# Performance work log

Hardware: AMD Instinct MI355X
Metric: run time of the kernel (lower is better)

## Reference

```python
import jax, jax.numpy as jnp
import numpy as np

NUM_CLASSES = 80
TOP_K = 200
CONF_T = 0.05
NMS_T = 0.5
CROP = 300.0
A = 49104
B = 8
NEG = -1.0  # dead-score sentinel; real scores are sigmoid outputs in (0,1)


def setup_inputs() -> dict:
    key = jax.random.key(0)
    k1, k2, k3, k4, k5, k6 = jax.random.split(key, 6)
    # structured, plausible anchors in (ymin, xmin, ymax, xmax), pixel coords
    yc = jax.random.uniform(k1, (A,)) * CROP
    xc = jax.random.uniform(k2, (A,)) * CROP
    h = 10.0 + jax.random.uniform(k5, (A,)) * 90.0
    w = 10.0 + jax.random.uniform(k6, (A,)) * 90.0
    anchors = jnp.stack([yc - h / 2, xc - w / 2, yc + h / 2, xc + w / 2], axis=-1)
    confidences = jax.random.normal(k3, (B, A, NUM_CLASSES + 1), dtype=jnp.float32)
    regressions = jax.random.normal(k4, (B, A, 4), dtype=jnp.float32) * 0.1
    return {"confidences": confidences, "regressions": regressions, "anchors": anchors}


def _decode(regressions, anchors):
    yca = (anchors[:, 0] + anchors[:, 2]) / 2
    xca = (anchors[:, 1] + anchors[:, 3]) / 2
    ha = anchors[:, 2] - anchors[:, 0]
    wa = anchors[:, 3] - anchors[:, 1]
    w = jnp.exp(regressions[..., 3]) * wa
    h = jnp.exp(regressions[..., 2]) * ha
    yc = regressions[..., 0] * ha + yca
    xc = regressions[..., 1] * wa + xca
    # clamp exactly as the original: min-clamp on xmin/ymin, max-clamp on xmax/ymax
    xmin = jnp.maximum(xc - w / 2, 0.0) / CROP
    ymin = jnp.maximum(yc - h / 2, 0.0) / CROP
    xmax = jnp.minimum(xc + w / 2, CROP - 1.0) / CROP
    ymax = jnp.minimum(yc + h / 2, CROP - 1.0) / CROP
    return jnp.stack([xmin, ymin, xmax, ymax], axis=-1)  # [B,A,4] (x1,y1,x2,y2)


def _iou_one_to_many(box, boxes):
    x1 = jnp.maximum(box[0], boxes[:, 0])
    y1 = jnp.maximum(box[1], boxes[:, 1])
    x2 = jnp.minimum(box[2], boxes[:, 2])
    y2 = jnp.minimum(box[3], boxes[:, 3])
    inter = jnp.maximum(x2 - x1, 0.0) * jnp.maximum(y2 - y1, 0.0)
    area_b = (box[2] - box[0]) * (box[3] - box[1])
    areas = (boxes[:, 2] - boxes[:, 0]) * (boxes[:, 3] - boxes[:, 1])
    union = area_b + areas - inter
    return jnp.where(union > 0, inter / union, 0.0)


def _nms_image(boxes, probs):
    # boxes: [A,4], probs: [A,C] (sigmoid, background stripped)
    scores = jnp.max(probs, axis=1)
    classes = jnp.argmax(probs, axis=1)
    valid = scores > CONF_T
    # batched_nms trick: offset boxes per class so cross-class IoU is 0
    offset = classes.astype(boxes.dtype) * (jnp.max(boxes) + 1.0)
    boxes_o = boxes + offset[:, None]
    live = jnp.where(valid, scores, NEG)

    def body(live, _):
        idx = jnp.argmax(live)
        keep = live[idx] > 0.0
        iou = _iou_one_to_many(boxes_o[idx], boxes_o)
        live = jnp.where(keep & (iou > NMS_T), NEG, live)
        live = live.at[idx].set(NEG)
        return live, (idx, keep)

    _, (idxs, keeps) = jax.lax.scan(body, live, None, length=TOP_K)
    cls_k = classes[idxs]          # [TOP_K]
    sc_k = scores[idxs]            # [TOP_K]
    bx_k = boxes[idxs]             # [TOP_K,4]
    # per-class slot = rank among kept detections of the same class (keep order is score-descending)
    onehot = (cls_k[:, None] == jnp.arange(NUM_CLASSES)[None, :]) & keeps[:, None]
    slot = jnp.cumsum(onehot, axis=0)[jnp.arange(TOP_K), cls_k] - 1
    rows = jnp.where(keeps, cls_k + 1, NUM_CLASSES + 1)  # OOB row when dropped
    slot = jnp.where(keeps, slot, TOP_K)                 # OOB col when dropped
    vals = jnp.concatenate([sc_k[:, None], bx_k], axis=1)  # [TOP_K,5]
    out = jnp.zeros((NUM_CLASSES + 1, TOP_K, 5), boxes.dtype)
    return out.at[rows, slot].set(vals, mode="drop")


def reference(confidences, regressions, anchors):
    probs = jax.nn.sigmoid(confidences[:, :, 1:])
    boxes = _decode(regressions, anchors)
    return jax.vmap(_nms_image)(boxes, probs)  # [B, C+1, TOP_K, 5]
```

## Files before the change

### kernel.cpp

```cpp
#include <hip/hip_runtime.h>
#include <stdint.h>

#define NCLS 80
#define TOPK 200
#define CONF_T 0.05f
#define CROPF 300.0f
#define NA 49104
#define NB 8
#define NSEL 256
#define MKEYS 4096
#define APB 48
#define T1 192
#define CHUNK (APB * 81)
#define NGRP (NA / 16)
#define MROW 5
#define OUTFLO ((NCLS + 1) * TOPK * 5)
#define NBLK1 ((NB * NA) / APB)
#define BASE13 125542u
#define NBINS 4512

__device__ __forceinline__ void decode_box(const float4 rg, const float4 an,
                                           float& x1, float& y1, float& x2, float& y2) {
    float yca = (an.x + an.z) * 0.5f;
    float xca = (an.y + an.w) * 0.5f;
    float ha = an.z - an.x;
    float wa = an.w - an.y;
    float w = expf(rg.w) * wa;
    float h = expf(rg.z) * ha;
    float yc = rg.x * ha + yca;
    float xc = rg.y * wa + xca;
    x1 = fmaxf(xc - w * 0.5f, 0.0f) / CROPF;
    y1 = fmaxf(yc - h * 0.5f, 0.0f) / CROPF;
    x2 = fminf(xc + w * 0.5f, CROPF - 1.0f) / CROPF;
    y2 = fminf(yc + h * 0.5f, CROPF - 1.0f) / CROPF;
}

__device__ __forceinline__ float rlf(float v, int l) {
    return __int_as_float(__builtin_amdgcn_readlane(__float_as_int(v), l));
}

__global__ __launch_bounds__(T1) void phase1_kernel(
    const float* __restrict__ conf, const float* __restrict__ reg,
    const float* __restrict__ anch, float* __restrict__ scores,
    unsigned char* __restrict__ cls, float2* __restrict__ gm2,
    float* __restrict__ outz)
{
    __shared__ float lds[CHUNK];
    const int blk = blockIdx.x, t = threadIdx.x;

    {
        const int gid = blk * T1 + t;
        constexpr int TOT4 = NB * OUTFLO / 4;
        if (gid < TOT4)
            reinterpret_cast<float4*>(outz)[gid] = make_float4(0.f, 0.f, 0.f, 0.f);
    }

    const float4* src = reinterpret_cast<const float4*>(conf + (size_t)blk * CHUNK);
    float4* dst = reinterpret_cast<float4*>(lds);
    for (int i = t; i < CHUNK / 4; i += T1) dst[i] = src[i];
    __syncthreads();

    const int la = t >> 2, sub = t & 3;
    const int quad = blk * APB + la;
    const float* crow = lds + la * 81;
    float best = -3.0e38f; int bc = 255;
    #pragma unroll
    for (int k = 0; k < 20; ++k) {
        int c = 1 + sub + 4 * k;
        float v = crow[c];
        if (v > best) { best = v; bc = c; }
    }
    for (int m = 1; m <= 2; m <<= 1) {
        float ov = __shfl_xor(best, m);
        int oc = __shfl_xor(bc, m);
        if (ov > best || (ov == best && oc < bc)) { best = ov; bc = oc; }
    }
    float bmaxl = 0.0f;
    if (sub == 0) {
        scores[quad] = 1.0f / (1.0f + expf(-best));
        cls[quad] = (unsigned char)(bc - 1);
        int a = quad % NA;
        float4 rg = reinterpret_cast<const float4*>(reg)[quad];
        float4 an = reinterpret_cast<const float4*>(anch)[a];
        float x1, y1, x2, y2; decode_box(rg, an, x1, y1, x2, y2);
        bmaxl = fmaxf(fmaxf(x1, y1), fmaxf(x2, y2));
    }
    float wbest = best;
    #pragma unroll
    for (int m = 1; m < 64; m <<= 1) {
        wbest = fmaxf(wbest, __shfl_xor(wbest, m));
        bmaxl = fmaxf(bmaxl, __shfl_xor(bmaxl, m));
    }
    if ((t & 63) == 0)
        gm2[blk * 3 + (t >> 6)] = make_float2(1.0f / (1.0f + expf(-wbest)), bmaxl);
}

__device__ __forceinline__ void suffix_scan_1024(uint32_t v, int t,
                                                 uint32_t* wtot, uint32_t* outarr) {
    uint32_t r = v;
    const int lane = t & 63, w = t >> 6;
    #pragma unroll
    for (int m = 1; m < 64; m <<= 1) {
        uint32_t o = __shfl_down(r, m);
        if (lane + m < 64) r += o;
    }
    if (lane == 0) wtot[w] = r;
    __syncthreads();
    if (t < 16) {
        uint32_t v0 = wtot[t], x = v0;
        #pragma unroll
        for (int m = 1; m < 16; m <<= 1) {
            uint32_t o = __shfl_down(x, m);
            if (t + m < 16) x += o;
        }
        wtot[t] = x - v0;
    }
    __syncthreads();
    outarr[t] = r + wtot[w];
    __syncthreads();
}

__global__ __launch_bounds__(1024) void phase2_kernel(
    const float* __restrict__ reg, const float* __restrict__ anch,
    const float* __restrict__ scores, const unsigned char* __restrict__ cls,
    const float2* __restrict__ gm2, float* __restrict__ out)
{
    __shared__ uint64_t s_keys[MKEYS];
    __shared__ uint64_t s_skeys[MKEYS];
    __shared__ uint64_t s_mask[256 * MROW];
    __shared__ float4   s_boxo[256];
    __shared__ float    s_areao[256];
    __shared__ float    s_gm[NGRP + 3];
    __shared__ uint32_t s_glist[2048];
    __shared__ float4   s_keptbox[TOPK];
    __shared__ uint64_t s_clsmask[NCLS][4];
    __shared__ uint32_t s_ccount[NCLS];
    __shared__ uint32_t s_wtot[16];
    __shared__ uint32_t s_shv[12];
    __shared__ float    s_bmaxarr[16];
    __shared__ float    s_offm;
    __shared__ uint8_t  s_clsl[256];
    __shared__ uint64_t s_K[4], s_newK[4];
    __shared__ uint32_t s_chg;

    uint32_t* hist = (uint32_t*)s_keys;
    uint32_t* csum = (uint32_t*)s_skeys;

    const int b = blockIdx.x;
    const int t = threadIdx.x;

    for (int i = t; i < NBINS; i += 1024) hist[i] = 0;
    if (t < 12) s_shv[t] = 0;
    __syncthreads();

    {
        const float2* gmb = gm2 + (size_t)b * NGRP;
        float wm = 0.0f;
        for (int i = t; i < NGRP; i += 1024) {
            float2 v = gmb[i];
            s_gm[i] = v.x;
            wm = fmaxf(wm, v.y);
            if (v.x > CONF_T) {
                int ib = (int)((__float_as_uint(v.x) >> 13) - BASE13);
                ib = max(0, min(NBINS - 1, ib));
                atomicAdd(&hist[ib], 1u);
            }
        }
        #pragma unroll
        for (int m = 1; m < 64; m <<= 1) wm = fmaxf(wm, __shfl_xor(wm, m));
        if ((t & 63) == 0) s_bmaxarr[t >> 6] = wm;
    }
    __syncthreads();

    uint32_t v8 = 0;
    if (t * 8 < NBINS) {
        #pragma unroll
        for (int k = 0; k < 8; ++k) v8 += hist[t * 8 + k];
    }
    suffix_scan_1024(v8, t, s_wtot, csum);
    {
        uint32_t sIn = csum[t];
        uint32_t sNext = (t == 1023) ? 0u : csum[t + 1];
        if (sIn >= NSEL && sNext < NSEL) { s_shv[0] = (uint32_t)t; s_shv[1] = sNext; s_shv[2] = 1; }
    }
    __syncthreads();
    if (t == 0) {
        float mx = s_bmaxarr[0];
        #pragma unroll
        for (int k = 1; k < 16; ++k) mx = fmaxf(mx, s_bmaxarr[k]);
        s_offm = mx + 1.0f;
        if (s_shv[2]) {
            uint32_t chunk = s_shv[0], run2 = s_shv[1]; int cb = -1;
            for (int k = 7; k >= 0; --k) {
                uint32_t v = hist[chunk * 8 + k];
                if (cb < 0 && run2 + v >= NSEL) cb = (int)(chunk * 8 + k);
                run2 += v;
            }
            s_shv[3] = BASE13 + (uint32_t)cb;
        } else s_shv[3] = 0;
    }
    __syncthreads();

    const uint32_t T13 = s_shv[3];
    for (int i = t; i < NGRP; i += 1024) {
        float s = s_gm[i];
        if (s > CONF_T && (__float_as_uint(s) >> 13) >= T13) {
            uint32_t p = atomicAdd(&s_shv[8], 1u);
            if (p < 2048u) s_glist[p] = (uint32_t)i;
        }
    }
    __syncthreads();
    uint32_t ngl = s_shv[8]; if (ngl > 2048u) ngl = 2048u;

    {
        const float4* sc4 = reinterpret_cast<const float4*>(scores + (size_t)b * NA);
        #define GATH1(s, g) { if ((s) > CONF_T) { uint32_t _b = __float_as_uint(s); \
            if ((_b >> 13) >= T13) { uint32_t _p = atomicAdd(&s_shv[4], 1u); \
                if (_p < MKEYS) s_keys[_p] = ((uint64_t)_b << 32) | \
                    (uint64_t)(0xFFFFFFFFu - (uint32_t)(g)); } } }
        for (int idx = t; idx < (int)(ngl * 4); idx += 1024) {
            uint32_t gi = s_glist[idx >> 2];
            int q = idx & 3;
            float4 s4 = sc4[gi * 4 + q];
            uint32_t g0 = gi * 16 + (uint32_t)q * 4;
            GATH1(s4.x, g0)     GATH1(s4.y, g0 + 1)
            GATH1(s4.z, g0 + 2) GATH1(s4.w, g0 + 3)
        }
    }
    __syncthreads();
    uint32_t nGa = s_shv[4]; if (nGa > MKEYS) nGa = MKEYS;
    const int lim = (nGa < 256u) ? (int)nGa : 256;

    {
        const int lane = t & 63;
        const uint32_t nch = (nGa + 63) >> 6;
        for (int s = 0; s < 4; ++s) {
            int kid = t + s * 1024;
            bool act = kid < (int)nGa;
            if (__ballot(act) == 0ull) continue;
            uint64_t my = act ? s_keys[kid] : ~0ull;
            uint32_t r = 0;
            for (uint32_t ch = 0; ch < nch; ++ch) {
                uint32_t src = ch * 64 + (uint32_t)lane;
                uint64_t kc = (src < nGa) ? s_keys[src] : 0ull;
                uint32_t clo = (uint32_t)kc, chi = (uint32_t)(kc >> 32);
                for (int jj = 0; jj < 64; ++jj) {
                    uint32_t olo = (uint32_t)__builtin_amdgcn_readlane((int)clo, jj);
                    uint32_t ohi = (uint32_t)__builtin_amdgcn_readlane((int)chi, jj);
                    uint64_t ok = ((uint64_t)ohi << 32) | olo;
                    r += (ok > my) ? 1u : 0u;
                }
            }
            if (act) s_skeys[r] = my;
        }
    }
    __syncthreads();

    const float offm = s_offm;
    if (t < 256) {
        if (t < lim) {
            uint64_t key = s_skeys[t];
            uint32_t g = 0xFFFFFFFFu - (uint32_t)key;
            size_t qi = (size_t)b * NA + g;
            int c = (int)cls[qi];
            s_clsl[t] = (uint8_t)c;
            float4 rg = reinterpret_cast<const float4*>(reg)[qi];
            float4 an = reinterpret_cast<const float4*>(anch)[g];
            float x1, y1, x2, y2; decode_box(rg, an, x1, y1, x2, y2);
            float off = (float)c * offm;
            float4 bo = make_float4(x1 + off, y1 + off, x2 + off, y2 + off);
            s_boxo[t] = bo;
            s_areao[t] = (bo.z - bo.x) * (bo.w - bo.y);
        } else {
            s_clsl[t] = 0;
            s_boxo[t] = make_float4(0.f, 0.f, 0.f, 0.f);
            s_areao[t] = 0.f;
        }
    }
    if (t < 4) {
        int lo = t * 64, n = lim - lo;
        s_K[t] = (n >= 64) ? ~0ull : (n > 0 ? ((~0ull) >> (64 - n)) : 0ull);
    }
    if (t < NCLS * 4) ((uint64_t*)s_clsmask)[t] = 0ull;
    __syncthreads();

    {
        const int wv = t >> 6, lane = t & 63;
        const int rbase = (wv & 3) * 64, c = wv >> 2;
        const int i = rbase + lane;
        float4 bi = s_boxo[i];
        float aI = s_areao[i];
        float4 vj = s_boxo[c * 64 + lane];
        float vA = s_areao[c * 64 + lane];
        uint64_t m = 0ull;
        for (int jj = 0; jj < 64; ++jj) {
            float bx1 = rlf(vj.x, jj), by1 = rlf(vj.y, jj);
            float bx2 = rlf(vj.z, jj), by2 = rlf(vj.w, jj);
            float aJ  = rlf(vA, jj);
            float ix1 = fmaxf(bi.x, bx1), iy1 = fmaxf(bi.y, by1);
            float ix2 = fminf(bi.z, bx2), iy2 = fminf(bi.w, by2);
            float inter = fmaxf(ix2 - ix1, 0.f) * fmaxf(iy2 - iy1, 0.f);
            float uni = aI + aJ - inter;
            if (uni > 0.f && inter + inter > uni) m |= (1ull << jj);
        }
        s_mask[(size_t)i * MROW + c] = m;
    }
    __syncthreads();

    {
        const int jw = (t >> 6) & 3, jb = t & 63;
        const uint64_t below = (jb == 0) ? 0ull : ((~0ull) >> (64 - jb));
        const uint64_t* mrow = s_mask + (size_t)(t & 255) * MROW;
        for (int round = 0; round < 300; ++round) {
            bool nb = false;
            if (t < 256) {
                uint64_t dead = 0ull;
                #pragma unroll
                for (int w = 0; w < 4; ++w) {
                    uint64_t mm = mrow[w] & s_K[w];
                    if (w < jw) dead |= mm;
                    else if (w == jw) dead |= (mm & below);
                }
                nb = (dead == 0ull) && (t < lim);
            }
            uint64_t bal = __ballot(nb);
            if (t < 256 && (t & 63) == 0) s_newK[jw] = bal;
            if (t == 0) s_chg = 0;
            __syncthreads();
            if (t < 4 && s_newK[t] != s_K[t]) atomicOr(&s_chg, 1u);
            __syncthreads();
            if (!s_chg) break;
            if (t < 4) s_K[t] = s_newK[t];
            __syncthreads();
        }
    }

    if (t < 256 && ((s_K[(t >> 6) & 3] >> (t & 63)) & 1ull))
        atomicOr(&s_clsmask[s_clsl[t]][(t >> 6) & 3], 1ull << (t & 63));
    __syncthreads();
    if (t < NCLS) {
        uint32_t n = 0;
        #pragma unroll
        for (int w = 0; w < 4; ++w) n += (uint32_t)__popcll(s_clsmask[t][w]);
        s_ccount[t] = n;
    }
    if (t == 0) {
        uint32_t n = 0;
        #pragma unroll
        for (int w = 0; w < 4; ++w) n += (uint32_t)__popcll(s_K[w]);
        s_shv[7] = n;
    }
    __syncthreads();

    {
        const int jw = (t >> 6) & 3, jb = t & 63;
        bool kept = (t < 256) && ((s_K[jw] >> jb) & 1ull);
        if (kept) {
            const uint64_t below = (jb == 0) ? 0ull : ((~0ull) >> (64 - jb));
            uint32_t ord = (uint32_t)__popcll(s_K[jw] & below);
            for (int w = 0; w < jw; ++w) ord += (uint32_t)__popcll(s_K[w]);
            if (ord < TOPK) {
                int c = (int)s_clsl[t];
                const uint64_t* cm = s_clsmask[c];
                uint32_t slot = (uint32_t)__popcll(cm[jw] & below);
                for (int w = 0; w < jw; ++w) slot += (uint32_t)__popcll(cm[w]);
                uint64_t key = s_skeys[t];
                uint32_t g = 0xFFFFFFFFu - (uint32_t)key;
                float scv = __uint_as_float((uint32_t)(key >> 32));
                size_t qi = (size_t)b * NA + g;
                float4 rg = reinterpret_cast<const float4*>(reg)[qi];
                float4 an = reinterpret_cast<const float4*>(anch)[g];
                float x1, y1, x2, y2; decode_box(rg, an, x1, y1, x2, y2);
                float* o = out + (((size_t)b * (NCLS + 1) + (size_t)(c + 1)) * TOPK + slot) * 5;
                o[0] = scv; o[1] = x1; o[2] = y1; o[3] = x2; o[4] = y2;
                s_keptbox[ord] = s_boxo[t];
            }
        }
    }
    __syncthreads();

    if (t == 0) {
        uint32_t nk = s_shv[7];
        if (nk < TOPK && nGa > (uint32_t)lim) {
            for (uint32_t ci = (uint32_t)lim; ci < nGa && nk < TOPK; ++ci) {
                uint64_t key = s_skeys[ci];
                uint32_t g = 0xFFFFFFFFu - (uint32_t)key;
                size_t qi = (size_t)b * NA + g;
                int c = (int)cls[qi];
                float4 rg = reinterpret_cast<const float4*>(reg)[qi];
                float4 an = reinterpret_cast<const float4*>(anch)[g];
                float x1, y1, x2, y2; decode_box(rg, an, x1, y1, x2, y2);
                float off = (float)c * offm;
                float4 bo = make_float4(x1 + off, y1 + off, x2 + off, y2 + off);
                float aB2 = (bo.z - bo.x) * (bo.w - bo.y);
                bool sup = false;
                for (uint32_t k2 = 0; k2 < nk && !sup; ++k2) {
                    float4 kb = s_keptbox[k2];
                    float aK = (kb.z - kb.x) * (kb.w - kb.y);
                    float ix1 = fmaxf(bo.x, kb.x), iy1 = fmaxf(bo.y, kb.y);
                    float ix2 = fminf(bo.z, kb.z), iy2 = fminf(bo.w, kb.w);
                    float inter = fmaxf(ix2 - ix1, 0.f) * fmaxf(iy2 - iy1, 0.f);
                    float uni = aB2 + aK - inter;
                    sup = (uni > 0.f && inter + inter > uni);
                }
                if (!sup) {
                    uint32_t slot = s_ccount[c]; s_ccount[c] = slot + 1;
                    float scv = __uint_as_float((uint32_t)(key >> 32));
                    float* o = out + (((size_t)b * (NCLS + 1) + (size_t)(c + 1)) * TOPK + slot) * 5;
                    o[0] = scv; o[1] = x1; o[2] = y1; o[3] = x2; o[4] = y2;
                    s_keptbox[nk] = bo;
                    ++nk;
                }
            }
        }
    }
}

extern "C" void kernel_launch(void* const* d_in, const int* in_sizes, int n_in,
                              void* d_out, int out_size, void* d_ws, size_t ws_size,
                              hipStream_t stream)
{
    const float* conf = (const float*)d_in[0];
    const float* reg  = (const float*)d_in[1];
    const float* anch = (const float*)d_in[2];
    float* out = (float*)d_out;

    char* ws = (char*)d_ws;
    float* scores = (float*)ws;
    float2* gm2 = (float2*)(ws + (size_t)NB * NA * 4);
    unsigned char* cls = (unsigned char*)(ws + (size_t)NB * NA * 4
                                             + (size_t)NB * NGRP * 8);

    phase1_kernel<<<NBLK1, T1, 0, stream>>>(conf, reg, anch, scores, cls, gm2, out);
    phase2_kernel<<<NB, 1024, 0, stream>>>(reg, anch, scores, cls, gm2, out);
}
```

Measured before the change: 63.64 us.

## Precompute packed sort keys and decoded boxes in phase 1; single-wave NMS fixpoint

```diff
diff --git a/kernel.cpp b/kernel.cpp
--- a/kernel.cpp
+++ b/kernel.cpp
@@ -4,13 +4,14 @@
 #define NCLS 80
 #define TOPK 200
 #define CONF_T 0.05f
+#define CONF_BITS 0x3D4CCCCDu
 #define CROPF 300.0f
 #define NA 49104
 #define NB 8
 #define NSEL 256
 #define MKEYS 4096
-#define APB 48
-#define T1 192
+#define APB 64
+#define T1 256
 #define CHUNK (APB * 81)
 #define NGRP (NA / 16)
 #define MROW 5
@@ -41,8 +42,8 @@
 
 __global__ __launch_bounds__(T1) void phase1_kernel(
     const float* __restrict__ conf, const float* __restrict__ reg,
-    const float* __restrict__ anch, float* __restrict__ scores,
-    unsigned char* __restrict__ cls, float2* __restrict__ gm2,
+    const float* __restrict__ anch, unsigned long long* __restrict__ key64,
+    float4* __restrict__ boxes, float2* __restrict__ gm2,
     float* __restrict__ outz)
 {
     __shared__ float lds[CHUNK];
@@ -75,15 +76,25 @@
         int oc = __shfl_xor(bc, m);
         if (ov > best || (ov == best && oc < bc)) { best = ov; bc = oc; }
     }
+    unsigned long long key = 0ull;
     float bmaxl = 0.0f;
     if (sub == 0) {
-        scores[quad] = 1.0f / (1.0f + expf(-best));
-        cls[quad] = (unsigned char)(bc - 1);
         int a = quad % NA;
+        float s = 1.0f / (1.0f + expf(-best));
+        uint32_t ginv = 0x1FFFFu - (uint32_t)a;
+        key = ((unsigned long long)__float_as_uint(s) << 32)
+            | (unsigned long long)((ginv << 7) | (uint32_t)(bc - 1));
         float4 rg = reinterpret_cast<const float4*>(reg)[quad];
         float4 an = reinterpret_cast<const float4*>(anch)[a];
         float x1, y1, x2, y2; decode_box(rg, an, x1, y1, x2, y2);
+        boxes[quad] = make_float4(x1, y1, x2, y2);
         bmaxl = fmaxf(fmaxf(x1, y1), fmaxf(x2, y2));
+    }
+    {
+        const int lane = t & 63, w = t >> 6;
+        unsigned long long kk = __shfl(key, (lane & 15) * 4);
+        if (lane < 16)
+            key64[(size_t)blk * APB + w * 16 + lane] = kk;
     }
     float wbest = best;
     #pragma unroll
@@ -92,7 +103,7 @@
         bmaxl = fmaxf(bmaxl, __shfl_xor(bmaxl, m));
     }
     if ((t & 63) == 0)
-        gm2[blk * 3 + (t >> 6)] = make_float2(1.0f / (1.0f + expf(-wbest)), bmaxl);
+        gm2[blk * 4 + (t >> 6)] = make_float2(1.0f / (1.0f + expf(-wbest)), bmaxl);
 }
 
 __device__ __forceinline__ void suffix_scan_1024(uint32_t v, int t,
@@ -121,14 +132,14 @@
 }
 
 __global__ __launch_bounds__(1024) void phase2_kernel(
-    const float* __restrict__ reg, const float* __restrict__ anch,
-    const float* __restrict__ scores, const unsigned char* __restrict__ cls,
+    const unsigned long long* __restrict__ key64, const float4* __restrict__ boxes,
     const float2* __restrict__ gm2, float* __restrict__ out)
 {
     __shared__ uint64_t s_keys[MKEYS];
     __shared__ uint64_t s_skeys[MKEYS];
     __shared__ uint64_t s_mask[256 * MROW];
     __shared__ float4   s_boxo[256];
+    __shared__ float4   s_braw[256];
     __shared__ float    s_areao[256];
     __shared__ float    s_gm[NGRP + 3];
     __shared__ uint32_t s_glist[2048];
@@ -140,8 +151,7 @@
     __shared__ float    s_bmaxarr[16];
     __shared__ float    s_offm;
     __shared__ uint8_t  s_clsl[256];
-    __shared__ uint64_t s_K[4], s_newK[4];
-    __shared__ uint32_t s_chg;
+    __shared__ uint64_t s_K[4];
 
     uint32_t* hist = (uint32_t*)s_keys;
     uint32_t* csum = (uint32_t*)s_skeys;
@@ -213,18 +223,15 @@
     uint32_t ngl = s_shv[8]; if (ngl > 2048u) ngl = 2048u;
 
     {
-        const float4* sc4 = reinterpret_cast<const float4*>(scores + (size_t)b * NA);
-        #define GATH1(s, g) { if ((s) > CONF_T) { uint32_t _b = __float_as_uint(s); \
-            if ((_b >> 13) >= T13) { uint32_t _p = atomicAdd(&s_shv[4], 1u); \
-                if (_p < MKEYS) s_keys[_p] = ((uint64_t)_b << 32) | \
-                    (uint64_t)(0xFFFFFFFFu - (uint32_t)(g)); } } }
-        for (int idx = t; idx < (int)(ngl * 4); idx += 1024) {
-            uint32_t gi = s_glist[idx >> 2];
-            int q = idx & 3;
-            float4 s4 = sc4[gi * 4 + q];
-            uint32_t g0 = gi * 16 + (uint32_t)q * 4;
-            GATH1(s4.x, g0)     GATH1(s4.y, g0 + 1)
-            GATH1(s4.z, g0 + 2) GATH1(s4.w, g0 + 3)
+        const unsigned long long* kb = key64 + (size_t)b * NA;
+        for (int idx = t; idx < (int)(ngl * 16); idx += 1024) {
+            uint32_t gi = s_glist[idx >> 4];
+            unsigned long long key = kb[gi * 16 + (idx & 15)];
+            uint32_t bits = (uint32_t)(key >> 32);
+            if (bits > CONF_BITS && (bits >> 13) >= T13) {
+                uint32_t p = atomicAdd(&s_shv[4], 1u);
+                if (p < MKEYS) s_keys[p] = key;
+            }
         }
     }
     __syncthreads();
@@ -260,26 +267,22 @@
     if (t < 256) {
         if (t < lim) {
             uint64_t key = s_skeys[t];
-            uint32_t g = 0xFFFFFFFFu - (uint32_t)key;
-            size_t qi = (size_t)b * NA + g;
-            int c = (int)cls[qi];
+            uint32_t low = (uint32_t)key;
+            int c = (int)(low & 0x7Fu);
+            uint32_t g = 0x1FFFFu - (low >> 7);
             s_clsl[t] = (uint8_t)c;
-            float4 rg = reinterpret_cast<const float4*>(reg)[qi];
-            float4 an = reinterpret_cast<const float4*>(anch)[g];
-            float x1, y1, x2, y2; decode_box(rg, an, x1, y1, x2, y2);
+            float4 br = boxes[(size_t)b * NA + g];
+            s_braw[t] = br;
             float off = (float)c * offm;
-            float4 bo = make_float4(x1 + off, y1 + off, x2 + off, y2 + off);
+            float4 bo = make_float4(br.x + off, br.y + off, br.z + off, br.w + off);
             s_boxo[t] = bo;
             s_areao[t] = (bo.z - bo.x) * (bo.w - bo.y);
         } else {
             s_clsl[t] = 0;
+            s_braw[t] = make_float4(0.f, 0.f, 0.f, 0.f);
             s_boxo[t] = make_float4(0.f, 0.f, 0.f, 0.f);
             s_areao[t] = 0.f;
         }
-    }
-    if (t < 4) {
-        int lo = t * 64, n = lim - lo;
-        s_K[t] = (n >= 64) ? ~0ull : (n > 0 ? ((~0ull) >> (64 - n)) : 0ull);
     }
     if (t < NCLS * 4) ((uint64_t*)s_clsmask)[t] = 0ull;
     __syncthreads();
@@ -307,33 +310,43 @@
     }
     __syncthreads();
 
-    {
-        const int jw = (t >> 6) & 3, jb = t & 63;
-        const uint64_t below = (jb == 0) ? 0ull : ((~0ull) >> (64 - jb));
-        const uint64_t* mrow = s_mask + (size_t)(t & 255) * MROW;
-        for (int round = 0; round < 300; ++round) {
-            bool nb = false;
-            if (t < 256) {
+    if (t < 64) {
+        const int lane = t;
+        uint64_t mr[4][4];
+        #pragma unroll
+        for (int wr = 0; wr < 4; ++wr)
+            #pragma unroll
+            for (int wc = 0; wc < 4; ++wc)
+                mr[wr][wc] = s_mask[(size_t)(wr * 64 + lane) * MROW + wc];
+        const uint64_t below = (lane == 0) ? 0ull : ((~0ull) >> (64 - lane));
+        uint64_t K[4];
+        #pragma unroll
+        for (int w = 0; w < 4; ++w) {
+            int lo = w * 64, n = lim - lo;
+            K[w] = (n >= 64) ? ~0ull : (n > 0 ? ((~0ull) >> (64 - n)) : 0ull);
+        }
+        for (int round = 0; round < 257; ++round) {
+            uint64_t nK[4];
+            #pragma unroll
+            for (int wr = 0; wr < 4; ++wr) {
                 uint64_t dead = 0ull;
                 #pragma unroll
                 for (int w = 0; w < 4; ++w) {
-                    uint64_t mm = mrow[w] & s_K[w];
-                    if (w < jw) dead |= mm;
-                    else if (w == jw) dead |= (mm & below);
+                    uint64_t mm = mr[wr][w] & K[w];
+                    if (w < wr) dead |= mm;
+                    else if (w == wr) dead |= (mm & below);
                 }
-                nb = (dead == 0ull) && (t < lim);
-            }
-            uint64_t bal = __ballot(nb);
-            if (t < 256 && (t & 63) == 0) s_newK[jw] = bal;
-            if (t == 0) s_chg = 0;
-            __syncthreads();
-            if (t < 4 && s_newK[t] != s_K[t]) atomicOr(&s_chg, 1u);
-            __syncthreads();
-            if (!s_chg) break;
-            if (t < 4) s_K[t] = s_newK[t];
-            __syncthreads();
-        }
-    }
+                bool nb = (dead == 0ull) && (wr * 64 + lane < lim);
+                nK[wr] = __ballot(nb);
+            }
+            bool same = (nK[0] == K[0]) && (nK[1] == K[1]) &&
+                        (nK[2] == K[2]) && (nK[3] == K[3]);
+            K[0] = nK[0]; K[1] = nK[1]; K[2] = nK[2]; K[3] = nK[3];
+            if (same) break;
+        }
+        if (lane < 4) s_K[lane] = K[lane];
+    }
+    __syncthreads();
 
     if (t < 256 && ((s_K[(t >> 6) & 3] >> (t & 63)) & 1ull))
         atomicOr(&s_clsmask[s_clsl[t]][(t >> 6) & 3], 1ull << (t & 63));
@@ -364,15 +377,10 @@
                 const uint64_t* cm = s_clsmask[c];
                 uint32_t slot = (uint32_t)__popcll(cm[jw] & below);
                 for (int w = 0; w < jw; ++w) slot += (uint32_t)__popcll(cm[w]);
-                uint64_t key = s_skeys[t];
-                uint32_t g = 0xFFFFFFFFu - (uint32_t)key;
-                float scv = __uint_as_float((uint32_t)(key >> 32));
-                size_t qi = (size_t)b * NA + g;
-                float4 rg = reinterpret_cast<const float4*>(reg)[qi];
-                float4 an = reinterpret_cast<const float4*>(anch)[g];
-                float x1, y1, x2, y2; decode_box(rg, an, x1, y1, x2, y2);
+                float scv = __uint_as_float((uint32_t)(s_skeys[t] >> 32));
+                float4 br = s_braw[t];
                 float* o = out + (((size_t)b * (NCLS + 1) + (size_t)(c + 1)) * TOPK + slot) * 5;
-                o[0] = scv; o[1] = x1; o[2] = y1; o[3] = x2; o[4] = y2;
+                o[0] = scv; o[1] = br.x; o[2] = br.y; o[3] = br.z; o[4] = br.w;
                 s_keptbox[ord] = s_boxo[t];
             }
         }
@@ -384,14 +392,12 @@
         if (nk < TOPK && nGa > (uint32_t)lim) {
             for (uint32_t ci = (uint32_t)lim; ci < nGa && nk < TOPK; ++ci) {
                 uint64_t key = s_skeys[ci];
-                uint32_t g = 0xFFFFFFFFu - (uint32_t)key;
-                size_t qi = (size_t)b * NA + g;
-                int c = (int)cls[qi];
-                float4 rg = reinterpret_cast<const float4*>(reg)[qi];
-                float4 an = reinterpret_cast<const float4*>(anch)[g];
-                float x1, y1, x2, y2; decode_box(rg, an, x1, y1, x2, y2);
+                uint32_t low = (uint32_t)key;
+                int c = (int)(low & 0x7Fu);
+                uint32_t g = 0x1FFFFu - (low >> 7);
+                float4 br = boxes[(size_t)b * NA + g];
                 float off = (float)c * offm;
-                float4 bo = make_float4(x1 + off, y1 + off, x2 + off, y2 + off);
+                float4 bo = make_float4(br.x + off, br.y + off, br.z + off, br.w + off);
                 float aB2 = (bo.z - bo.x) * (bo.w - bo.y);
                 bool sup = false;
                 for (uint32_t k2 = 0; k2 < nk && !sup; ++k2) {
@@ -407,7 +413,7 @@
                     uint32_t slot = s_ccount[c]; s_ccount[c] = slot + 1;
                     float scv = __uint_as_float((uint32_t)(key >> 32));
                     float* o = out + (((size_t)b * (NCLS + 1) + (size_t)(c + 1)) * TOPK + slot) * 5;
-                    o[0] = scv; o[1] = x1; o[2] = y1; o[3] = x2; o[4] = y2;
+                    o[0] = scv; o[1] = br.x; o[2] = br.y; o[3] = br.z; o[4] = br.w;
                     s_keptbox[nk] = bo;
                     ++nk;
                 }
@@ -426,11 +432,10 @@
     float* out = (float*)d_out;
 
     char* ws = (char*)d_ws;
-    float* scores = (float*)ws;
-    float2* gm2 = (float2*)(ws + (size_t)NB * NA * 4);
-    unsigned char* cls = (unsigned char*)(ws + (size_t)NB * NA * 4
-                                             + (size_t)NB * NGRP * 8);
-
-    phase1_kernel<<<NBLK1, T1, 0, stream>>>(conf, reg, anch, scores, cls, gm2, out);
-    phase2_kernel<<<NB, 1024, 0, stream>>>(reg, anch, scores, cls, gm2, out);
-}
+    unsigned long long* key64 = (unsigned long long*)ws;
+    float4* boxes = (float4*)(ws + (size_t)NB * NA * 8);
+    float2* gm2 = (float2*)(ws + (size_t)NB * NA * 24);
+
+    phase1_kernel<<<NBLK1, T1, 0, stream>>>(conf, reg, anch, key64, boxes, gm2, out);
+    phase2_kernel<<<NB, 1024, 0, stream>>>(key64, boxes, gm2, out);
+}
```

Measured after the change: 63.82 us. No clear change (+0.3%).
